# Performance work log

Measured on AMD Instinct MI355X. Metric: run time of the kernel, lower is better.

Reference implementation:

```python
import jax, jax.numpy as jnp
import numpy as np

B, T, U, D = 2, 256, 64, 512
INNER, VOCAB = 512, 4096


def setup_inputs() -> dict:
    key = jax.random.key(0)
    k1, k2, k3, k4, k5, k6 = jax.random.split(key, 6)
    s1 = 1.0 / np.sqrt(2 * D)      # torch Linear init scale for fan_in=2D
    s2 = 1.0 / np.sqrt(INNER)
    return {
        "enc_state": jax.random.normal(k1, (B, T, D), dtype=jnp.float32),
        "dec_state": jax.random.normal(k2, (B, U, D), dtype=jnp.float32),
        "W1": jax.random.normal(k3, (INNER, 2 * D), dtype=jnp.float32) * s1,
        "b1": jax.random.normal(k4, (INNER,), dtype=jnp.float32) * s1,
        "W2": jax.random.normal(k5, (VOCAB, INNER), dtype=jnp.float32) * s2,
        "b2": jax.random.normal(k6, (VOCAB,), dtype=jnp.float32) * s2,
    }


def reference(enc_state, dec_state, W1, b1, W2, b2):
    # JointNet: repeat enc (B,T,1,D)->(B,T,U,D), dec (B,1,U,D)->(B,T,U,D),
    # concat -> Linear(2D,inner) -> tanh -> Linear(inner,vocab).
    # Equivalent efficient form: split W1 into enc/dec halves, project each
    # sequence once, broadcast-add (the concat+Linear decomposes exactly).
    d = enc_state.shape[-1]
    We, Wd = W1[:, :d], W1[:, d:]
    enc_proj = jnp.einsum("btd,id->bti", enc_state, We)   # (B,T,inner)
    dec_proj = jnp.einsum("bud,id->bui", dec_state, Wd)   # (B,U,inner)
    h = jnp.tanh(enc_proj[:, :, None, :] + dec_proj[:, None, :, :] + b1)  # (B,T,U,inner)
    logits = jnp.einsum("btui,vi->btuv", h, W2) + b2       # (B,T,U,vocab)
    return logits
```

## Files before the change

kernel.cpp:

```cpp
#include <hip/hip_runtime.h>
#include <hip/hip_bf16.h>
#include <stdint.h>

#define T_DIM 256
#define U_DIM 64
#define D_DIM 512
#define NIN 512
#define NV 4096

typedef __bf16 bf16x8 __attribute__((ext_vector_type(8)));
typedef float f32x4 __attribute__((ext_vector_type(4)));

static __device__ __forceinline__ unsigned short f2bf(float x) {
  union { float f; unsigned int u; } v; v.f = x;
  unsigned int r = v.u + 0x7FFFu + ((v.u >> 16) & 1u);
  return (unsigned short)(r >> 16);
}

static __device__ __forceinline__ void gload_lds16(const unsigned short* g, void* l) {
  __builtin_amdgcn_global_load_lds(
      (__attribute__((address_space(1))) void*)(unsigned short*)g,
      (__attribute__((address_space(3))) void*)l, 16, 0, 0);
}

__global__ __launch_bounds__(256) void convert_w2_kernel(const float* __restrict__ W2,
                                                         unsigned short* __restrict__ W2b) {
  int q = blockIdx.x * 256 + threadIdx.x;
  const float4 v0 = *(const float4*)(W2 + (size_t)q * 8);
  const float4 v1 = *(const float4*)(W2 + (size_t)q * 8 + 4);
  union { unsigned short s[8]; uint4 u; } o;
  o.s[0] = f2bf(v0.x); o.s[1] = f2bf(v0.y); o.s[2] = f2bf(v0.z); o.s[3] = f2bf(v0.w);
  o.s[4] = f2bf(v1.x); o.s[5] = f2bf(v1.y); o.s[6] = f2bf(v1.z); o.s[7] = f2bf(v1.w);
  *(uint4*)(W2b + (size_t)q * 8) = o.u;
}

__global__ __launch_bounds__(256) void proj_kernel(const float* __restrict__ enc,
                                                   const float* __restrict__ dec,
                                                   const float* __restrict__ W1,
                                                   float* __restrict__ ep0,
                                                   float* __restrict__ ep1,
                                                   float* __restrict__ dp0,
                                                   float* __restrict__ dp1) {
  __shared__ unsigned short As[128 * 32];
  __shared__ unsigned short Bs[128 * 32];
  const int tid = threadIdx.x;
  const int tile_m = blockIdx.x >> 3;
  const int kh = (blockIdx.x >> 2) & 1;
  const int tile_n = blockIdx.x & 3;
  const bool is_dec = (tile_m == 4);
  const float* X = is_dec ? dec : enc;
  const int xrow0 = is_dec ? 0 : tile_m * 128;
  const int wcol0 = is_dec ? D_DIM : 0;
  float* outp = is_dec ? (kh ? dp1 : dp0) : (kh ? ep1 : ep0);

  const int lane = tid & 63;
  const int wv = tid >> 6;
  const int wr = wv >> 1, wc = wv & 1;

  const int arow = tid >> 1;
  const int acol = (tid & 1) * 16;

  f32x4 acc[4][4] = {};

  const float* pa = X + (size_t)(xrow0 + arow) * D_DIM + acol;
  const float* pb = W1 + (size_t)(tile_n * 128 + arow) * (2 * D_DIM) + wcol0 + acol;

  for (int k0 = kh * 256; k0 < kh * 256 + 256; k0 += 32) {
    float4 av0 = *(const float4*)(pa + k0);
    float4 av1 = *(const float4*)(pa + k0 + 4);
    float4 av2 = *(const float4*)(pa + k0 + 8);
    float4 av3 = *(const float4*)(pa + k0 + 12);
    float4 bv0 = *(const float4*)(pb + k0);
    float4 bv1 = *(const float4*)(pb + k0 + 4);
    float4 bv2 = *(const float4*)(pb + k0 + 8);
    float4 bv3 = *(const float4*)(pb + k0 + 12);
    __syncthreads();
    union { unsigned short s[8]; uint4 u; } u0, u1, w0, w1;
    u0.s[0] = f2bf(av0.x); u0.s[1] = f2bf(av0.y); u0.s[2] = f2bf(av0.z); u0.s[3] = f2bf(av0.w);
    u0.s[4] = f2bf(av1.x); u0.s[5] = f2bf(av1.y); u0.s[6] = f2bf(av1.z); u0.s[7] = f2bf(av1.w);
    u1.s[0] = f2bf(av2.x); u1.s[1] = f2bf(av2.y); u1.s[2] = f2bf(av2.z); u1.s[3] = f2bf(av2.w);
    u1.s[4] = f2bf(av3.x); u1.s[5] = f2bf(av3.y); u1.s[6] = f2bf(av3.z); u1.s[7] = f2bf(av3.w);
    w0.s[0] = f2bf(bv0.x); w0.s[1] = f2bf(bv0.y); w0.s[2] = f2bf(bv0.z); w0.s[3] = f2bf(bv0.w);
    w0.s[4] = f2bf(bv1.x); w0.s[5] = f2bf(bv1.y); w0.s[6] = f2bf(bv1.z); w0.s[7] = f2bf(bv1.w);
    w1.s[0] = f2bf(bv2.x); w1.s[1] = f2bf(bv2.y); w1.s[2] = f2bf(bv2.z); w1.s[3] = f2bf(bv2.w);
    w1.s[4] = f2bf(bv3.x); w1.s[5] = f2bf(bv3.y); w1.s[6] = f2bf(bv3.z); w1.s[7] = f2bf(bv3.w);
    *(uint4*)&As[arow * 32 + acol] = u0.u;
    *(uint4*)&As[arow * 32 + acol + 8] = u1.u;
    *(uint4*)&Bs[arow * 32 + acol] = w0.u;
    *(uint4*)&Bs[arow * 32 + acol + 8] = w1.u;
    __syncthreads();
    bf16x8 af[4], bff[4];
#pragma unroll
    for (int mi = 0; mi < 4; ++mi)
      af[mi] = *(const bf16x8*)&As[(wr * 64 + mi * 16 + (lane & 15)) * 32 + (lane >> 4) * 8];
#pragma unroll
    for (int ni = 0; ni < 4; ++ni)
      bff[ni] = *(const bf16x8*)&Bs[(wc * 64 + ni * 16 + (lane & 15)) * 32 + (lane >> 4) * 8];
#pragma unroll
    for (int mi = 0; mi < 4; ++mi)
#pragma unroll
      for (int ni = 0; ni < 4; ++ni)
        acc[mi][ni] = __builtin_amdgcn_mfma_f32_16x16x32_bf16(af[mi], bff[ni], acc[mi][ni], 0, 0, 0);
  }

#pragma unroll
  for (int mi = 0; mi < 4; ++mi) {
#pragma unroll
    for (int r = 0; r < 4; ++r) {
      int row = xrow0 + wr * 64 + mi * 16 + ((lane >> 4) << 2) + r;
      float* po = outp + (size_t)row * NIN + tile_n * 128 + wc * 64 + (lane & 15);
#pragma unroll
      for (int ni = 0; ni < 4; ++ni) po[ni * 16] = acc[mi][ni][r];
    }
  }
}

__global__ __launch_bounds__(256) void h_kernel(const float* __restrict__ ep0,
                                                const float* __restrict__ ep1,
                                                const float* __restrict__ dp0,
                                                const float* __restrict__ dp1,
                                                const float* __restrict__ b1,
                                                unsigned short* __restrict__ Hb) {
  int q = blockIdx.x * 256 + threadIdx.x;
  int m = q >> 6;
  int i0 = (q & 63) << 3;
  size_t eoff = (size_t)(m >> 6) * NIN + i0;
  size_t doff = (size_t)((m >> 14) * U_DIM + (m & 63)) * NIN + i0;
  float4 e0 = *(const float4*)(ep0 + eoff);
  float4 e1 = *(const float4*)(ep0 + eoff + 4);
  float4 f0 = *(const float4*)(ep1 + eoff);
  float4 f1 = *(const float4*)(ep1 + eoff + 4);
  float4 d0 = *(const float4*)(dp0 + doff);
  float4 d1 = *(const float4*)(dp0 + doff + 4);
  float4 g0 = *(const float4*)(dp1 + doff);
  float4 g1 = *(const float4*)(dp1 + doff + 4);
  float4 c0 = *(const float4*)(b1 + i0);
  float4 c1 = *(const float4*)(b1 + i0 + 4);
  float x[8] = { e0.x + f0.x + d0.x + g0.x + c0.x, e0.y + f0.y + d0.y + g0.y + c0.y,
                 e0.z + f0.z + d0.z + g0.z + c0.z, e0.w + f0.w + d0.w + g0.w + c0.w,
                 e1.x + f1.x + d1.x + g1.x + c1.x, e1.y + f1.y + d1.y + g1.y + c1.y,
                 e1.z + f1.z + d1.z + g1.z + c1.z, e1.w + f1.w + d1.w + g1.w + c1.w };
  union { unsigned short s[8]; uint4 u; } o;
#pragma unroll
  for (int j = 0; j < 8; ++j) {
    float ex = __expf(2.0f * x[j]);
    float t = 1.0f - 2.0f / (ex + 1.0f);
    o.s[j] = f2bf(t);
  }
  *(uint4*)(Hb + (size_t)q * 8) = o.u;
}

__global__ __launch_bounds__(512, 2) void gemm256_kernel(const unsigned short* __restrict__ Hb,
                                                         const unsigned short* __restrict__ W2b,
                                                         const float* __restrict__ b2,
                                                         float* __restrict__ out) {
  __shared__ __align__(16) char smem[131072];
  const int tid = threadIdx.x;
  const int bid = blockIdx.x;
  const int swz = ((bid & 7) << 8) | (bid >> 3);
  const int tile_n = swz & 15, tile_m = swz >> 4;
  const int m0 = tile_m * 256, n0 = tile_n * 256;
  const int lane = tid & 63, w = tid >> 6;
  const int wr = w >> 2, wc = w & 3;

  const int srow0 = (w << 4) + (lane >> 2);
  const int segp = ((((lane & 3) - ((lane >> 3) & 3)) & 3) << 3);
  const unsigned short* pA0 = Hb + (size_t)(m0 + srow0) * 512 + segp;
  const unsigned short* pA1 = pA0 + 128 * 512;
  const unsigned short* pB0 = W2b + (size_t)(n0 + srow0) * 512 + segp;
  const unsigned short* pB1 = pB0 + 128 * 512;
  const int dstOff = (w << 10) + (lane << 4);
  const int laneA = ((lane & 15) << 6) + ((((lane >> 4) + ((lane >> 1) & 7)) & 3) << 4);
  const int wrOff = wr << 13;
  const int wcOff = wc << 12;

  f32x4 acc[8][4] = {};
  bf16x8 af[8], bq0, bq1;

#define STAGE_A(BUF, KH, T) do { \
    gload_lds16(pA0 + (T) * 64 + (KH) * 32, smem + (BUF) * 32768 + (KH) * 16384 + dstOff); \
    gload_lds16(pA1 + (T) * 64 + (KH) * 32, smem + (BUF) * 32768 + (KH) * 16384 + 8192 + dstOff); \
  } while (0)
#define STAGE_B(BUF, KH, T) do { \
    gload_lds16(pB0 + (T) * 64 + (KH) * 32, smem + 65536 + (BUF) * 32768 + (KH) * 16384 + dstOff); \
    gload_lds16(pB1 + (T) * 64 + (KH) * 32, smem + 65536 + (BUF) * 32768 + (KH) * 16384 + 8192 + dstOff); \
  } while (0)
#define DS_A(BUF, KH, MI) (*(const bf16x8*)(smem + (BUF) * 32768 + (KH) * 16384 + wrOff + (MI) * 1024 + laneA))
#define DS_B(BUF, KH, NI) (*(const bf16x8*)(smem + 65536 + (BUF) * 32768 + (KH) * 16384 + wcOff + (NI) * 1024 + laneA))
#define LD_A(BUF, KH) do { \
    _Pragma("unroll") for (int mi = 0; mi < 8; ++mi) af[mi] = DS_A(BUF, KH, mi); \
  } while (0)
#define QUAD(NH) do { \
    __builtin_amdgcn_s_setprio(1); \
    _Pragma("unroll") for (int mi = 0; mi < 8; ++mi) { \
      acc[mi][2 * (NH)]     = __builtin_amdgcn_mfma_f32_16x16x32_bf16(af[mi], bq0, acc[mi][2 * (NH)], 0, 0, 0); \
      acc[mi][2 * (NH) + 1] = __builtin_amdgcn_mfma_f32_16x16x32_bf16(af[mi], bq1, acc[mi][2 * (NH) + 1], 0, 0, 0); \
    } \
    __builtin_amdgcn_s_setprio(0); \
  } while (0)
#define BAR() __builtin_amdgcn_s_barrier()
#define LGKM0() asm volatile("s_waitcnt lgkmcnt(0)" ::: "memory")
#define VMCNT4() asm volatile("s_waitcnt vmcnt(4)" ::: "memory")
#define VMCNT0() asm volatile("s_waitcnt vmcnt(0)" ::: "memory")

  STAGE_A(0, 0, 0); STAGE_A(0, 1, 0); STAGE_B(0, 0, 0); STAGE_B(0, 1, 0);
  STAGE_A(1, 0, 1); STAGE_B(1, 0, 1);
  VMCNT4();
  BAR();

  for (int i = 0; i < 3; ++i) {
    const int t1 = 2 * i + 1, t2 = 2 * i + 2, t3 = 2 * i + 3;
    LD_A(0, 0); bq0 = DS_B(0, 0, 0); bq1 = DS_B(0, 0, 1);
    STAGE_A(1, 1, t1);
    BAR(); LGKM0(); QUAD(0); BAR();
    bq0 = DS_B(0, 0, 2); bq1 = DS_B(0, 0, 3);
    STAGE_B(1, 1, t1);
    BAR(); LGKM0(); QUAD(1); BAR();
    LD_A(0, 1); bq0 = DS_B(0, 1, 0); bq1 = DS_B(0, 1, 1);
    STAGE_A(0, 0, t2);
    BAR(); LGKM0(); QUAD(0); BAR();
    bq0 = DS_B(0, 1, 2); bq1 = DS_B(0, 1, 3);
    STAGE_B(0, 0, t2);
    VMCNT4();
    BAR(); LGKM0(); QUAD(1); BAR();
    LD_A(1, 0); bq0 = DS_B(1, 0, 0); bq1 = DS_B(1, 0, 1);
    STAGE_A(0, 1, t2);
    BAR(); LGKM0(); QUAD(0); BAR();
    bq0 = DS_B(1, 0, 2); bq1 = DS_B(1, 0, 3);
    STAGE_B(0, 1, t2);
    BAR(); LGKM0(); QUAD(1); BAR();
    LD_A(1, 1); bq0 = DS_B(1, 1, 0); bq1 = DS_B(1, 1, 1);
    STAGE_A(1, 0, t3);
    BAR(); LGKM0(); QUAD(0); BAR();
    bq0 = DS_B(1, 1, 2); bq1 = DS_B(1, 1, 3);
    STAGE_B(1, 0, t3);
    VMCNT4();
    BAR(); LGKM0(); QUAD(1); BAR();
  }

  LD_A(0, 0); bq0 = DS_B(0, 0, 0); bq1 = DS_B(0, 0, 1);
  STAGE_A(1, 1, 7);
  BAR(); LGKM0(); QUAD(0); BAR();
  bq0 = DS_B(0, 0, 2); bq1 = DS_B(0, 0, 3);
  STAGE_B(1, 1, 7);
  BAR(); LGKM0(); QUAD(1); BAR();
  LD_A(0, 1); bq0 = DS_B(0, 1, 0); bq1 = DS_B(0, 1, 1);
  BAR(); LGKM0(); QUAD(0); BAR();
  bq0 = DS_B(0, 1, 2); bq1 = DS_B(0, 1, 3);
  VMCNT0();
  BAR(); LGKM0(); QUAD(1); BAR();
  LD_A(1, 0); bq0 = DS_B(1, 0, 0); bq1 = DS_B(1, 0, 1);
  BAR(); LGKM0(); QUAD(0); BAR();
  bq0 = DS_B(1, 0, 2); bq1 = DS_B(1, 0, 3);
  BAR(); LGKM0(); QUAD(1); BAR();
  LD_A(1, 1); bq0 = DS_B(1, 1, 0); bq1 = DS_B(1, 1, 1);
  BAR(); LGKM0(); QUAD(0); BAR();
  bq0 = DS_B(1, 1, 2); bq1 = DS_B(1, 1, 3);
  BAR(); LGKM0(); QUAD(1);

  float b2v[4];
#pragma unroll
  for (int ni = 0; ni < 4; ++ni) b2v[ni] = b2[n0 + wc * 64 + ni * 16 + (lane & 15)];
#pragma unroll
  for (int mi = 0; mi < 8; ++mi) {
#pragma unroll
    for (int r = 0; r < 4; ++r) {
      int row = m0 + wr * 128 + mi * 16 + ((lane >> 4) << 2) + r;
      float* po = out + (size_t)row * NV + n0 + wc * 64 + (lane & 15);
#pragma unroll
      for (int ni = 0; ni < 4; ++ni) po[ni * 16] = acc[mi][ni][r] + b2v[ni];
    }
  }
#undef STAGE_A
#undef STAGE_B
#undef DS_A
#undef DS_B
#undef LD_A
#undef QUAD
#undef BAR
#undef LGKM0
#undef VMCNT4
#undef VMCNT0
}

extern "C" void kernel_launch(void* const* d_in, const int* in_sizes, int n_in,
                              void* d_out, int out_size, void* d_ws, size_t ws_size,
                              hipStream_t stream) {
  const float* enc = (const float*)d_in[0];
  const float* dec = (const float*)d_in[1];
  const float* W1  = (const float*)d_in[2];
  const float* b1  = (const float*)d_in[3];
  const float* W2  = (const float*)d_in[4];
  const float* b2  = (const float*)d_in[5];
  float* out = (float*)d_out;

  char* ws = (char*)d_ws;
  unsigned short* W2b = (unsigned short*)(ws);
  float* ep0 = (float*)(ws + 4194304);
  float* ep1 = (float*)(ws + 5242880);
  float* dp0 = (float*)(ws + 6291456);
  float* dp1 = (float*)(ws + 6553600);
  unsigned short* Hb = (unsigned short*)(ws + 6815744);

  hipLaunchKernelGGL(convert_w2_kernel, dim3(1024), dim3(256), 0, stream, W2, W2b);
  hipLaunchKernelGGL(proj_kernel, dim3(40), dim3(256), 0, stream, enc, dec, W1, ep0, ep1, dp0, dp1);
  hipLaunchKernelGGL(h_kernel, dim3(8192), dim3(256), 0, stream, ep0, ep1, dp0, dp1, b1, Hb);
  hipLaunchKernelGGL(gemm256_kernel, dim3(2048), dim3(512), 0, stream, Hb, W2b, b2, out);
}
```

Before: 241.5 us.

## Merge W2 conversion with projection kernel, retile GEMM grid, use nontemporal stores

Folds the W2 bf16 conversion and the encoder/decoder projection into one launch, removing one kernel launch and letting the two independent jobs run side by side. Changes the GEMM block-to-tile mapping so each XCD works on a contiguous group of M tiles with 4x4 supertiles, aiming for better L2 reuse. Moves the b2 bias load before the main loop and writes the output with nontemporal stores to avoid polluting cache. The proj blocks now sit behind 1024 conversion blocks in dispatch order, which may delay the projection work.

New measurement: 240.2 us. Within noise of the previous version (-0.5%).

```diff
diff --git a/kernel.cpp b/kernel.cpp
--- a/kernel.cpp
+++ b/kernel.cpp
@@ -23,18 +23,9 @@
       (__attribute__((address_space(3))) void*)l, 16, 0, 0);
 }
 
-__global__ __launch_bounds__(256) void convert_w2_kernel(const float* __restrict__ W2,
-                                                         unsigned short* __restrict__ W2b) {
-  int q = blockIdx.x * 256 + threadIdx.x;
-  const float4 v0 = *(const float4*)(W2 + (size_t)q * 8);
-  const float4 v1 = *(const float4*)(W2 + (size_t)q * 8 + 4);
-  union { unsigned short s[8]; uint4 u; } o;
-  o.s[0] = f2bf(v0.x); o.s[1] = f2bf(v0.y); o.s[2] = f2bf(v0.z); o.s[3] = f2bf(v0.w);
-  o.s[4] = f2bf(v1.x); o.s[5] = f2bf(v1.y); o.s[6] = f2bf(v1.z); o.s[7] = f2bf(v1.w);
-  *(uint4*)(W2b + (size_t)q * 8) = o.u;
-}
-
-__global__ __launch_bounds__(256) void proj_kernel(const float* __restrict__ enc,
+__global__ __launch_bounds__(256) void prep_kernel(const float* __restrict__ W2,
+                                                   unsigned short* __restrict__ W2b,
+                                                   const float* __restrict__ enc,
                                                    const float* __restrict__ dec,
                                                    const float* __restrict__ W1,
                                                    float* __restrict__ ep0,
@@ -44,9 +35,22 @@
   __shared__ unsigned short As[128 * 32];
   __shared__ unsigned short Bs[128 * 32];
   const int tid = threadIdx.x;
-  const int tile_m = blockIdx.x >> 3;
-  const int kh = (blockIdx.x >> 2) & 1;
-  const int tile_n = blockIdx.x & 3;
+
+  if (blockIdx.x < 1024) {
+    int q = blockIdx.x * 256 + tid;
+    const float4 v0 = *(const float4*)(W2 + (size_t)q * 8);
+    const float4 v1 = *(const float4*)(W2 + (size_t)q * 8 + 4);
+    union { unsigned short s[8]; uint4 u; } o;
+    o.s[0] = f2bf(v0.x); o.s[1] = f2bf(v0.y); o.s[2] = f2bf(v0.z); o.s[3] = f2bf(v0.w);
+    o.s[4] = f2bf(v1.x); o.s[5] = f2bf(v1.y); o.s[6] = f2bf(v1.z); o.s[7] = f2bf(v1.w);
+    *(uint4*)(W2b + (size_t)q * 8) = o.u;
+    return;
+  }
+
+  const int pbid = blockIdx.x - 1024;
+  const int tile_m = pbid >> 3;
+  const int kh = (pbid >> 2) & 1;
+  const int tile_n = pbid & 3;
   const bool is_dec = (tile_m == 4);
   const float* X = is_dec ? dec : enc;
   const int xrow0 = is_dec ? 0 : tile_m * 128;
@@ -56,7 +60,6 @@
   const int lane = tid & 63;
   const int wv = tid >> 6;
   const int wr = wv >> 1, wc = wv & 1;
-
   const int arow = tid >> 1;
   const int acol = (tid & 1) * 16;
 
@@ -157,8 +160,12 @@
   __shared__ __align__(16) char smem[131072];
   const int tid = threadIdx.x;
   const int bid = blockIdx.x;
-  const int swz = ((bid & 7) << 8) | (bid >> 3);
-  const int tile_n = swz & 15, tile_m = swz >> 4;
+  const int xcd = bid & 7;
+  const int idx = bid >> 3;
+  const int sup = idx >> 4;
+  const int within = idx & 15;
+  const int tile_m = (xcd << 4) | ((sup >> 2) << 2) | (within >> 2);
+  const int tile_n = ((sup & 3) << 2) | (within & 3);
   const int m0 = tile_m * 256, n0 = tile_n * 256;
   const int lane = tid & 63, w = tid >> 6;
   const int wr = w >> 2, wc = w & 3;
@@ -170,12 +177,16 @@
   const unsigned short* pB0 = W2b + (size_t)(n0 + srow0) * 512 + segp;
   const unsigned short* pB1 = pB0 + 128 * 512;
   const int dstOff = (w << 10) + (lane << 4);
-  const int laneA = ((lane & 15) << 6) + ((((lane >> 4) + ((lane >> 1) & 7)) & 3) << 4);
+  const int laneA = ((lane & 15) << 6) | ((((lane >> 4) + ((lane >> 1) & 7)) & 3) << 4);
   const int wrOff = wr << 13;
   const int wcOff = wc << 12;
 
   f32x4 acc[8][4] = {};
   bf16x8 af[8], bq0, bq1;
+
+  float b2v[4];
+#pragma unroll
+  for (int ni = 0; ni < 4; ++ni) b2v[ni] = b2[n0 + wc * 64 + ni * 16 + (lane & 15)];
 
 #define STAGE_A(BUF, KH, T) do { \
     gload_lds16(pA0 + (T) * 64 + (KH) * 32, smem + (BUF) * 32768 + (KH) * 16384 + dstOff); \
@@ -258,9 +269,6 @@
   bq0 = DS_B(1, 1, 2); bq1 = DS_B(1, 1, 3);
   BAR(); LGKM0(); QUAD(1);
 
-  float b2v[4];
-#pragma unroll
-  for (int ni = 0; ni < 4; ++ni) b2v[ni] = b2[n0 + wc * 64 + ni * 16 + (lane & 15)];
 #pragma unroll
   for (int mi = 0; mi < 8; ++mi) {
 #pragma unroll
@@ -268,7 +276,8 @@
       int row = m0 + wr * 128 + mi * 16 + ((lane >> 4) << 2) + r;
       float* po = out + (size_t)row * NV + n0 + wc * 64 + (lane & 15);
 #pragma unroll
-      for (int ni = 0; ni < 4; ++ni) po[ni * 16] = acc[mi][ni][r] + b2v[ni];
+      for (int ni = 0; ni < 4; ++ni)
+        __builtin_nontemporal_store(acc[mi][ni][r] + b2v[ni], po + ni * 16);
     }
   }
 #undef STAGE_A
@@ -302,8 +311,8 @@
   float* dp1 = (float*)(ws + 6553600);
   unsigned short* Hb = (unsigned short*)(ws + 6815744);
 
-  hipLaunchKernelGGL(convert_w2_kernel, dim3(1024), dim3(256), 0, stream, W2, W2b);
-  hipLaunchKernelGGL(proj_kernel, dim3(40), dim3(256), 0, stream, enc, dec, W1, ep0, ep1, dp0, dp1);
+  hipLaunchKernelGGL(prep_kernel, dim3(1064), dim3(256), 0, stream,
+                     W2, W2b, enc, dec, W1, ep0, ep1, dp0, dp1);
   hipLaunchKernelGGL(h_kernel, dim3(8192), dim3(256), 0, stream, ep0, ep1, dp0, dp1, b1, Hb);
   hipLaunchKernelGGL(gemm256_kernel, dim3(2048), dim3(512), 0, stream, Hb, W2b, b2, out);
 }
```
